# Performance work log

Measured on AMD Instinct MI355X. Metric: run time of the kernel, lower is better.

## Reference

```python
import jax, jax.numpy as jnp
import numpy as np

N, F, H, C, E = 50000, 256, 256, 40, 800000
CURV = 1.0
EPS = 4e-3      # hgcn PoincareBall eps for float32
MIN_NORM = 1e-15


def setup_inputs() -> dict:
    key = jax.random.key(0)
    ks = jax.random.split(key, 8)
    return {
        "x": jax.random.normal(ks[0], (N, F), jnp.float32),
        "edge_index": jax.random.randint(ks[1], (2, E), 0, N, dtype=jnp.int64),
        "Wl0": jax.random.normal(ks[2], (F, H), jnp.float32) / np.sqrt(F).astype(np.float32),
        "bl0": jnp.zeros((H,), jnp.float32),
        "Wr0": jax.random.normal(ks[3], (F, H), jnp.float32) / np.sqrt(F).astype(np.float32),
        "Wl1": jax.random.normal(ks[4], (H, C), jnp.float32) / np.sqrt(H).astype(np.float32),
        "bl1": jnp.zeros((C,), jnp.float32),
        "Wr1": jax.random.normal(ks[5], (H, C), jnp.float32) / np.sqrt(H).astype(np.float32),
        "W_lin": jax.random.normal(ks[6], (C * C, C), jnp.float32) / np.sqrt(C * C).astype(np.float32),
        "b_lin": jnp.zeros((C,), jnp.float32),
    }


def _sage(x, src, dst, Wl, bl, Wr):
    # PyG SAGEConv (mean aggr): lin_l(mean_{j->i} x_j) + lin_r(x_i), lin_l has bias
    msg = jax.ops.segment_sum(x[src], dst, num_segments=N)          # [N, d]
    cnt = jax.ops.segment_sum(jnp.ones((src.shape[0],), x.dtype), dst, num_segments=N)
    mean = msg / jnp.maximum(cnt, 1.0)[:, None]
    return mean @ Wl + bl + x @ Wr


def _proj(x, c):
    norm = jnp.maximum(jnp.linalg.norm(x, axis=-1, keepdims=True), MIN_NORM)
    maxnorm = (1.0 - EPS) / jnp.sqrt(c)
    return jnp.where(norm > maxnorm, x / norm * maxnorm, x)


def _logmap0(p, c):
    sqrt_c = jnp.sqrt(c)
    p_norm = jnp.maximum(jnp.linalg.norm(p, axis=-1, keepdims=True), MIN_NORM)
    arg = jnp.clip(sqrt_c * p_norm, -1.0 + 1e-6, 1.0 - 1e-6)
    return jnp.arctanh(arg) / (sqrt_c * p_norm) * p


def _expmap0(u, c):
    sqrt_c = jnp.sqrt(c)
    u_norm = jnp.maximum(jnp.linalg.norm(u, axis=-1, keepdims=True), MIN_NORM)
    return jnp.tanh(sqrt_c * u_norm) * u / (sqrt_c * u_norm)


def reference(x, edge_index, Wl0, bl0, Wr0, Wl1, bl1, Wr1, W_lin, b_lin):
    c = CURV
    src, dst = edge_index[0], edge_index[1]
    h = jax.nn.relu(_sage(x, src, dst, Wl0, bl0, Wr0))              # [N, H]
    h = _sage(h, src, dst, Wl1, bl1, Wr1)                            # [N, C]
    outer = jnp.einsum('ni,nj->nij', h, h).reshape(N, C * C)        # rank-1 outer, flattened
    h_hyp = _proj(outer, c)
    h_euc = _logmap0(h_hyp, c)                                       # proj_tan0 is identity
    h_euc = h_euc @ W_lin + b_lin                                    # [N, C]
    h_hyp = _proj(_expmap0(h_euc, c), c)
    return jax.nn.log_softmax(h_hyp, axis=-1)
```

## Files before the change

kernel.cpp:

```cpp
#include <hip/hip_runtime.h>
#include <math.h>


typedef short bf16x8 __attribute__((ext_vector_type(8)));
typedef float f32x4 __attribute__((ext_vector_type(4)));

#define AS1 __attribute__((address_space(1)))
#define AS3 __attribute__((address_space(3)))

__device__ inline unsigned pack_bf16_hu(float a, float b) {
    unsigned ua = __float_as_uint(a) + 0x8000u;
    unsigned ub = __float_as_uint(b) + 0x8000u;
    return __builtin_amdgcn_perm(ub, ua, 0x07060302u);
}

__device__ inline unsigned short f2bf_rne(float x) {
    unsigned u = __float_as_uint(x);
    unsigned r = (u + 0x7fffu + ((u >> 16) & 1u)) >> 16;
    return (unsigned short)r;
}

__device__ inline void split2(float a, float b, unsigned* hw, unsigned* lw) {
    unsigned ua = __float_as_uint(a) + 0x8000u;
    unsigned ub = __float_as_uint(b) + 0x8000u;
    *hw = __builtin_amdgcn_perm(ub, ua, 0x07060302u);
    float ra = a - __uint_as_float(ua & 0xFFFF0000u);
    float rb = b - __uint_as_float(ub & 0xFFFF0000u);
    unsigned va = __float_as_uint(ra) + 0x8000u;
    unsigned vb = __float_as_uint(rb) + 0x8000u;
    *lw = __builtin_amdgcn_perm(vb, va, 0x07060302u);
}


__global__ void k_count(const int* __restrict__ dst, int* __restrict__ deg, int E) {
    int e = blockIdx.x * 256 + threadIdx.x;
    if (e < E) atomicAdd(&deg[dst[e]], 1);
}

__global__ __launch_bounds__(256) void k_scanA(const int* __restrict__ deg,
                                               int* __restrict__ offs,
                                               float* __restrict__ invc,
                                               int* __restrict__ bsum, int N) {
    __shared__ int wt[4];
    int tid = threadIdx.x, lane = tid & 63, wid = tid >> 6;
    int base = blockIdx.x * 1024 + tid * 4;
    int v[4];
    #pragma unroll
    for (int j = 0; j < 4; ++j) {
        int i = base + j;
        v[j] = (i < N) ? deg[i] : 0;
        if (i < N) invc[i] = 1.0f / (float)max(v[j], 1);
    }
    int t = v[0] + v[1] + v[2] + v[3];
    int s = t;
    #pragma unroll
    for (int d = 1; d < 64; d <<= 1) {
        int u = __shfl_up(s, d);
        if (lane >= d) s += u;
    }
    if (lane == 63) wt[wid] = s;
    __syncthreads();
    int wpre = 0, btot = 0;
    #pragma unroll
    for (int q = 0; q < 4; ++q) {
        int x = wt[q];
        btot += x;
        if (q < wid) wpre += x;
    }
    int run = wpre + s - t;
    #pragma unroll
    for (int j = 0; j < 4; ++j) {
        int i = base + j;
        if (i < N) offs[i] = run;
        run += v[j];
    }
    if (tid == 0) bsum[blockIdx.x] = btot;
}

__global__ __launch_bounds__(64) void k_scanB(int* __restrict__ bsum,
                                              int* __restrict__ offs, int N, int G) {
    int lane = threadIdx.x;
    int run = 0;
    for (int base = 0; base < G; base += 64) {
        int i = base + lane;
        int v = (i < G) ? bsum[i] : 0;
        int s = v;
        #pragma unroll
        for (int d = 1; d < 64; d <<= 1) {
            int u = __shfl_up(s, d);
            if (lane >= d) s += u;
        }
        int tot = __shfl(s, 63);
        if (i < G) bsum[i] = run + s - v;
        run += tot;
    }
    if (lane == 0) offs[N] = run;
}

__global__ __launch_bounds__(256) void k_scanC(int* __restrict__ offs,
                                               const int* __restrict__ bsum, int N) {
    int add = bsum[blockIdx.x];
    int base = blockIdx.x * 1024 + threadIdx.x * 4;
    #pragma unroll
    for (int j = 0; j < 4; ++j) {
        int i = base + j;
        if (i < N) offs[i] += add;
    }
}

__global__ void k_scatter(const int* __restrict__ src, const int* __restrict__ dst,
                          const int* __restrict__ offs, int* __restrict__ cursor,
                          int* __restrict__ ssrc, int E) {
    int e = blockIdx.x * 256 + threadIdx.x;
    if (e >= E) return;
    int d = dst[e];
    int pos = offs[d] + atomicAdd(&cursor[d], 1);
    ssrc[pos] = src[e];
}


__global__ __launch_bounds__(256) void k_wsplit0(const float* __restrict__ Wl,
                                                 const float* __restrict__ Wr,
                                                 unsigned short* __restrict__ Bfh,
                                                 unsigned short* __restrict__ Bfl) {
    int idx = blockIdx.x * 256 + threadIdx.x;
    int lane = idx & 63;
    int nf = (idx >> 6) & 3;
    int g  = (idx >> 8) & 7;
    int w  = (idx >> 11) & 7;
    int ml = lane & 15, quad = lane >> 4;
    int wc = w & 3;
    int n = (w < 4) ? (wc * 64 + (nf & 2) * 16 + 2 * ml + (nf & 1))
                    : (256 + wc * 64 + nf * 16 + ml);
    int kbase = g * 32 + quad * 8;
    unsigned short h8[8], l8[8];
    #pragma unroll
    for (int e = 0; e < 8; ++e) {
        int k = kbase + e;
        float v = (n < 256) ? Wl[k * 256 + n] : Wr[k * 256 + (n - 256)];
        unsigned short h = f2bf_rne(v);
        float hf = __uint_as_float(((unsigned)h) << 16);
        h8[e] = h;
        l8[e] = f2bf_rne(v - hf);
    }
    *(uint4*)&Bfh[(size_t)idx * 8] = *(uint4*)h8;
    *(uint4*)&Bfl[(size_t)idx * 8] = *(uint4*)l8;
}


__global__ __launch_bounds__(256) void k_wsplit1(const float* __restrict__ Wl,
                                                 const float* __restrict__ Wr,
                                                 unsigned short* __restrict__ Bfh,
                                                 unsigned short* __restrict__ Bfl) {
    int idx = blockIdx.x * 256 + threadIdx.x;
    if (idx >= 40 * 64) return;
    int lane = idx & 63;
    int slot = idx >> 6;
    int nf = slot % 5;
    int kc = slot / 5;
    int ml = lane & 15, quad = lane >> 4;
    int n = nf * 16 + ml;
    int kbase = kc * 32 + quad * 8;
    unsigned short h8[8], l8[8];
    #pragma unroll
    for (int e = 0; e < 8; ++e) {
        int k = kbase + e;
        float v = (n < 40) ? Wl[k * 40 + n] : Wr[k * 40 + (n - 40)];
        unsigned short h = f2bf_rne(v);
        float hf = __uint_as_float(((unsigned)h) << 16);
        h8[e] = h;
        l8[e] = f2bf_rne(v - hf);
    }
    *(uint4*)&Bfh[(size_t)idx * 8] = *(uint4*)h8;
    *(uint4*)&Bfl[(size_t)idx * 8] = *(uint4*)l8;
}


__global__ __launch_bounds__(256) void k_xsplit(const float* __restrict__ X,
                                                unsigned short* __restrict__ Xh,
                                                unsigned short* __restrict__ Xl,
                                                int N) {
    int idx = blockIdx.x * 256 + threadIdx.x;
    int n = idx >> 5, c = idx & 31;
    float4 v0 = make_float4(0.f, 0.f, 0.f, 0.f);
    float4 v1 = make_float4(0.f, 0.f, 0.f, 0.f);
    if (n < N) {
        v0 = *(const float4*)&X[(size_t)n * 256 + c * 8];
        v1 = *(const float4*)&X[(size_t)n * 256 + c * 8 + 4];
    }
    unsigned h0, l0, h1, l1, h2, l2, h3, l3;
    split2(v0.x, v0.y, &h0, &l0);
    split2(v0.z, v0.w, &h1, &l1);
    split2(v1.x, v1.y, &h2, &l2);
    split2(v1.z, v1.w, &h3, &l3);
    int cp = c ^ (n & 7);
    size_t o = (size_t)n * 256 + cp * 8;
    *(uint4*)&Xh[o] = make_uint4(h0, h1, h2, h3);
    *(uint4*)&Xl[o] = make_uint4(l0, l1, l2, l3);
}


__global__ __launch_bounds__(512) void gemm0_mfma(const unsigned short* __restrict__ Xh,
                                                  const unsigned short* __restrict__ Xl,
                                                  const unsigned short* __restrict__ Bfh,
                                                  const unsigned short* __restrict__ Bfl,
                                                  unsigned short* __restrict__ Yl,
                                                  float* __restrict__ Yr, int N) {
    __shared__ __align__(16) unsigned short AhL[2][64 * 128];
    __shared__ __align__(16) unsigned short AlL[2][64 * 128];

    int tid = threadIdx.x;
    int lane = tid & 63;
    int w = __builtin_amdgcn_readfirstlane(tid >> 6);
    int ml = lane & 15, quad = lane >> 4;
    int m0 = blockIdx.x * 64;
    bool isYl = (w < 4);
    int wc = w & 3;

    auto stage = [&](int h) {
        #pragma unroll
        for (int j = 0; j < 2; ++j) {
            int idx = j * 512 + tid;
            int row = idx >> 4, c16 = idx & 15;
            size_t gsrc = (size_t)(m0 + row) * 512 + (size_t)h * 256 + c16 * 16;
            int loff = idx * 16;
            __builtin_amdgcn_global_load_lds((const AS1 unsigned*)((const char*)Xh + gsrc),
                                             (AS3 unsigned*)((char*)&AhL[h][0] + loff), 16, 0, 0);
            __builtin_amdgcn_global_load_lds((const AS1 unsigned*)((const char*)Xl + gsrc),
                                             (AS3 unsigned*)((char*)&AlL[h][0] + loff), 16, 0, 0);
        }
    };

    stage(0);

    f32x4 acc[4][4];
    #pragma unroll
    for (int a = 0; a < 4; ++a)
        #pragma unroll
        for (int b = 0; b < 4; ++b) acc[a][b] = (f32x4){0.f, 0.f, 0.f, 0.f};

    bf16x8 bh0[4], bl0[4], bh1[4], bl1[4];

    auto loadB = [&](int it, bf16x8* bh, bf16x8* bl) {
        size_t base = (((size_t)(w * 8 + it) * 4) * 64 + lane) * 8;
        #pragma unroll
        for (int nf = 0; nf < 4; ++nf) {
            bh[nf] = *(const bf16x8*)&Bfh[base + (size_t)nf * 512];
            bl[nf] = *(const bf16x8*)&Bfl[base + (size_t)nf * 512];
        }
    };

    loadB(0, bh0, bl0);
    __syncthreads();

    int swz = ml & 7;

    #pragma unroll
    for (int p = 0; p < 2; ++p) {
        if (p == 0) stage(1);
        const char* base_h = (const char*)&AhL[p][0];
        const char* base_l = (const char*)&AlL[p][0];
        #pragma unroll
        for (int g2 = 0; g2 < 4; ++g2) {
            int g = p * 4 + g2;
            bf16x8* bhc = (g & 1) ? bh1 : bh0;
            bf16x8* blc = (g & 1) ? bl1 : bl0;
            bf16x8* bhn = (g & 1) ? bh0 : bh1;
            bf16x8* bln = (g & 1) ? bl0 : bl1;
            if (g < 7) loadB(g + 1, bhn, bln);
            bf16x8 ah[4], al[4];
            #pragma unroll
            for (int mf = 0; mf < 4; ++mf) {
                int ro = (mf * 16 + ml) * 256 + (((g2 * 4 + quad) ^ swz) * 16);
                ah[mf] = *(const bf16x8*)(base_h + ro);
                al[mf] = *(const bf16x8*)(base_l + ro);
            }
            #pragma unroll
            for (int nf = 0; nf < 4; ++nf)
                #pragma unroll
                for (int mf = 0; mf < 4; ++mf) {
                    acc[mf][nf] = __builtin_amdgcn_mfma_f32_16x16x32_bf16(ah[mf], bhc[nf], acc[mf][nf], 0, 0, 0);
                    acc[mf][nf] = __builtin_amdgcn_mfma_f32_16x16x32_bf16(ah[mf], blc[nf], acc[mf][nf], 0, 0, 0);
                    acc[mf][nf] = __builtin_amdgcn_mfma_f32_16x16x32_bf16(al[mf], bhc[nf], acc[mf][nf], 0, 0, 0);
                }
        }
        if (p == 0) __syncthreads();
    }

    if (isYl) {
        #pragma unroll
        for (int mf = 0; mf < 4; ++mf)
            #pragma unroll
            for (int r = 0; r < 4; ++r) {
                int row = m0 + mf * 16 + quad * 4 + r;
                if (row < N) {
                    unsigned p0 = pack_bf16_hu(acc[mf][0][r], acc[mf][1][r]);
                    unsigned p1 = pack_bf16_hu(acc[mf][2][r], acc[mf][3][r]);
                    *(unsigned*)&Yl[(size_t)row * 256 + wc * 64 + 2 * ml] = p0;
                    *(unsigned*)&Yl[(size_t)row * 256 + wc * 64 + 32 + 2 * ml] = p1;
                }
            }
    } else {
        #pragma unroll
        for (int mf = 0; mf < 4; ++mf)
            #pragma unroll
            for (int r = 0; r < 4; ++r) {
                int row = m0 + mf * 16 + quad * 4 + r;
                if (row < N) {
                    #pragma unroll
                    for (int nf = 0; nf < 4; ++nf)
                        Yr[(size_t)row * 256 + wc * 64 + nf * 16 + ml] = acc[mf][nf][r];
                }
            }
    }
}


__global__ __launch_bounds__(256) void combine0(const unsigned short* __restrict__ Yl,
                                                const float* __restrict__ Yr,
                                                const int* __restrict__ offs,
                                                const int* __restrict__ ssrc,
                                                const float* __restrict__ invc,
                                                const float* __restrict__ bl0,
                                                unsigned short* __restrict__ Hh,
                                                unsigned short* __restrict__ Hl, int N) {
    int wv = threadIdx.x >> 6, lane = threadIdx.x & 63;
    int n = blockIdx.x * 4 + wv;
    if (n >= N) return;
    int e0 = offs[n], e1 = offs[n + 1];
    float4 acc = make_float4(0.f, 0.f, 0.f, 0.f);
    int e = e0;
    for (; e + 7 < e1; e += 8) {
        int s0 = ssrc[e],     s1 = ssrc[e + 1], s2 = ssrc[e + 2], s3 = ssrc[e + 3];
        int s4 = ssrc[e + 4], s5 = ssrc[e + 5], s6 = ssrc[e + 6], s7 = ssrc[e + 7];
        uint2 p0 = *(const uint2*)&Yl[(size_t)s0 * 256 + lane * 4];
        uint2 p1 = *(const uint2*)&Yl[(size_t)s1 * 256 + lane * 4];
        uint2 p2 = *(const uint2*)&Yl[(size_t)s2 * 256 + lane * 4];
        uint2 p3 = *(const uint2*)&Yl[(size_t)s3 * 256 + lane * 4];
        uint2 p4 = *(const uint2*)&Yl[(size_t)s4 * 256 + lane * 4];
        uint2 p5 = *(const uint2*)&Yl[(size_t)s5 * 256 + lane * 4];
        uint2 p6 = *(const uint2*)&Yl[(size_t)s6 * 256 + lane * 4];
        uint2 p7 = *(const uint2*)&Yl[(size_t)s7 * 256 + lane * 4];
        acc.x += ((__uint_as_float(p0.x << 16) + __uint_as_float(p1.x << 16)) +
                  (__uint_as_float(p2.x << 16) + __uint_as_float(p3.x << 16))) +
                 ((__uint_as_float(p4.x << 16) + __uint_as_float(p5.x << 16)) +
                  (__uint_as_float(p6.x << 16) + __uint_as_float(p7.x << 16)));
        acc.y += ((__uint_as_float(p0.x & 0xFFFF0000u) + __uint_as_float(p1.x & 0xFFFF0000u)) +
                  (__uint_as_float(p2.x & 0xFFFF0000u) + __uint_as_float(p3.x & 0xFFFF0000u))) +
                 ((__uint_as_float(p4.x & 0xFFFF0000u) + __uint_as_float(p5.x & 0xFFFF0000u)) +
                  (__uint_as_float(p6.x & 0xFFFF0000u) + __uint_as_float(p7.x & 0xFFFF0000u)));
        acc.z += ((__uint_as_float(p0.y << 16) + __uint_as_float(p1.y << 16)) +
                  (__uint_as_float(p2.y << 16) + __uint_as_float(p3.y << 16))) +
                 ((__uint_as_float(p4.y << 16) + __uint_as_float(p5.y << 16)) +
                  (__uint_as_float(p6.y << 16) + __uint_as_float(p7.y << 16)));
        acc.w += ((__uint_as_float(p0.y & 0xFFFF0000u) + __uint_as_float(p1.y & 0xFFFF0000u)) +
                  (__uint_as_float(p2.y & 0xFFFF0000u) + __uint_as_float(p3.y & 0xFFFF0000u))) +
                 ((__uint_as_float(p4.y & 0xFFFF0000u) + __uint_as_float(p5.y & 0xFFFF0000u)) +
                  (__uint_as_float(p6.y & 0xFFFF0000u) + __uint_as_float(p7.y & 0xFFFF0000u)));
    }
    for (; e + 3 < e1; e += 4) {
        int s0 = ssrc[e], s1 = ssrc[e + 1], s2 = ssrc[e + 2], s3 = ssrc[e + 3];
        uint2 p = *(const uint2*)&Yl[(size_t)s0 * 256 + lane * 4];
        uint2 q = *(const uint2*)&Yl[(size_t)s1 * 256 + lane * 4];
        uint2 v = *(const uint2*)&Yl[(size_t)s2 * 256 + lane * 4];
        uint2 t = *(const uint2*)&Yl[(size_t)s3 * 256 + lane * 4];
        acc.x += (__uint_as_float(p.x << 16) + __uint_as_float(q.x << 16)) +
                 (__uint_as_float(v.x << 16) + __uint_as_float(t.x << 16));
        acc.y += (__uint_as_float(p.x & 0xFFFF0000u) + __uint_as_float(q.x & 0xFFFF0000u)) +
                 (__uint_as_float(v.x & 0xFFFF0000u) + __uint_as_float(t.x & 0xFFFF0000u));
        acc.z += (__uint_as_float(p.y << 16) + __uint_as_float(q.y << 16)) +
                 (__uint_as_float(v.y << 16) + __uint_as_float(t.y << 16));
        acc.w += (__uint_as_float(p.y & 0xFFFF0000u) + __uint_as_float(q.y & 0xFFFF0000u)) +
                 (__uint_as_float(v.y & 0xFFFF0000u) + __uint_as_float(t.y & 0xFFFF0000u));
    }
    for (; e < e1; ++e) {
        int s0 = ssrc[e];
        uint2 p = *(const uint2*)&Yl[(size_t)s0 * 256 + lane * 4];
        acc.x += __uint_as_float(p.x << 16);
        acc.y += __uint_as_float(p.x & 0xFFFF0000u);
        acc.z += __uint_as_float(p.y << 16);
        acc.w += __uint_as_float(p.y & 0xFFFF0000u);
    }
    float ic = invc[n];
    float4 b = *(const float4*)&bl0[lane * 4];
    float4 yr = *(const float4*)&Yr[(size_t)n * 256 + lane * 4];
    float hx = fmaxf(acc.x * ic + b.x + yr.x, 0.f);
    float hy = fmaxf(acc.y * ic + b.y + yr.y, 0.f);
    float hz = fmaxf(acc.z * ic + b.z + yr.z, 0.f);
    float hw = fmaxf(acc.w * ic + b.w + yr.w, 0.f);
    unsigned h0, h1, l0, l1;
    split2(hx, hy, &h0, &l0);
    split2(hz, hw, &h1, &l1);
    size_t offH = (size_t)n * 256 + lane * 4;
    *(uint2*)&Hh[offH] = make_uint2(h0, h1);
    *(uint2*)&Hl[offH] = make_uint2(l0, l1);
}


__global__ __launch_bounds__(256) void gemm1_mfma(const unsigned short* __restrict__ Hh,
                                                  const unsigned short* __restrict__ Hl,
                                                  const unsigned short* __restrict__ Bfh,
                                                  const unsigned short* __restrict__ Bfl,
                                                  unsigned short* __restrict__ Zl,
                                                  float* __restrict__ Zr, int N, int numTiles) {
    int tid = threadIdx.x;
    int lane = tid & 63;
    int w = __builtin_amdgcn_readfirstlane(tid >> 6);
    int ml = lane & 15, quad = lane >> 4;
    int t = blockIdx.x * 4 + w;
    if (t >= numTiles) return;

    const unsigned short* ahp = Hh + (size_t)(t * 16 + ml) * 256 + quad * 8;
    const unsigned short* alp = Hl + (size_t)(t * 16 + ml) * 256 + quad * 8;

    f32x4 acc[5];
    #pragma unroll
    for (int b = 0; b < 5; ++b) acc[b] = (f32x4){0.f, 0.f, 0.f, 0.f};

    #pragma unroll
    for (int kc = 0; kc < 8; ++kc) {
        bf16x8 ah = *(const bf16x8*)&ahp[kc * 32];
        bf16x8 al = *(const bf16x8*)&alp[kc * 32];
        #pragma unroll
        for (int nf = 0; nf < 5; ++nf) {
            size_t bo = (((size_t)(kc * 5 + nf)) * 64 + lane) * 8;
            bf16x8 bh = *(const bf16x8*)&Bfh[bo];
            bf16x8 bl = *(const bf16x8*)&Bfl[bo];
            acc[nf] = __builtin_amdgcn_mfma_f32_16x16x32_bf16(ah, bh, acc[nf], 0, 0, 0);
            acc[nf] = __builtin_amdgcn_mfma_f32_16x16x32_bf16(ah, bl, acc[nf], 0, 0, 0);
            acc[nf] = __builtin_amdgcn_mfma_f32_16x16x32_bf16(al, bh, acc[nf], 0, 0, 0);
        }
    }
    #pragma unroll
    for (int r = 0; r < 4; ++r) {
        int n = t * 16 + quad * 4 + r;
        if (n < N) {
            #pragma unroll
            for (int nf = 0; nf < 5; ++nf) {
                int col = nf * 16 + ml;
                if (col < 40) Zl[(size_t)n * 40 + col] = f2bf_rne(acc[nf][r]);
                else Zr[(size_t)n * 40 + (col - 40)] = acc[nf][r];
            }
        }
    }
}


__global__ __launch_bounds__(256) void combine1(const unsigned short* __restrict__ Zl,
                                                const float* __restrict__ Zr,
                                                const int* __restrict__ offs,
                                                const int* __restrict__ ssrc,
                                                const float* __restrict__ invc,
                                                const float* __restrict__ bl1,
                                                float* __restrict__ H2, int N) {
    int wv = threadIdx.x >> 6, lane = threadIdx.x & 63;
    int n = blockIdx.x * 4 + wv;
    if (n >= N) return;
    if (lane >= 40) return;
    int e0 = offs[n], e1 = offs[n + 1];
    float acc = 0.f;
    int e = e0;
    for (; e + 1 < e1; e += 2) {
        int s0 = ssrc[e], s1 = ssrc[e + 1];
        unsigned a = Zl[(size_t)s0 * 40 + lane];
        unsigned b = Zl[(size_t)s1 * 40 + lane];
        acc += __uint_as_float(a << 16) + __uint_as_float(b << 16);
    }
    if (e < e1) {
        unsigned a = Zl[(size_t)ssrc[e] * 40 + lane];
        acc += __uint_as_float(a << 16);
    }
    float v = acc * invc[n] + bl1[lane] + Zr[(size_t)n * 40 + lane];
    H2[(size_t)n * 40 + lane] = v;
}


__global__ __launch_bounds__(256) void k_wprep(const float* __restrict__ W,
                                               unsigned short* __restrict__ WbF) {
    int idx = blockIdx.x * 256 + threadIdx.x;
    if (idx >= 180 * 64) return;
    int slot = idx >> 6, lane = idx & 63;
    int cf = slot % 3;
    int cs = slot / 3;
    int s = cs % 3;
    int c = cs / 3;
    int ml = lane & 15, quad = lane >> 4;
    int col = cf * 16 + ml;
    int kbase = c * 96 + s * 32 + quad * 8;
    unsigned short v8[8];
    #pragma unroll
    for (int e = 0; e < 8; ++e) {
        int kp = kbase + e;
        int i = kp / 48;
        int j = kp - i * 48;
        float v = 0.f;
        if (col < 40 && i < 40 && j < 40) v = W[((size_t)(i * 40 + j)) * 40 + col];
        v8[e] = f2bf_rne(v);
    }
    *(uint4*)&WbF[(size_t)idx * 8] = *(uint4*)v8;
}


__global__ __launch_bounds__(256, 1) void k_final_mfma(const float* __restrict__ H2,
                                                       const unsigned short* __restrict__ WbF,
                                                       const float* __restrict__ blin,
                                                       float* __restrict__ out, int N) {
    int tid = threadIdx.x;
    int m0 = blockIdx.x * 64;
    int lane = tid & 63;
    int w = __builtin_amdgcn_readfirstlane(tid >> 6);
    int ml = lane & 15;
    int quad = lane >> 4;
    int row = w * 16 + ml;
    int gn = m0 + row;

    float g[48];
    float s2 = 0.f;
    #pragma unroll
    for (int q4 = 0; q4 < 10; ++q4) {
        float4 v = make_float4(0.f, 0.f, 0.f, 0.f);
        if (gn < N) v = *(const float4*)&H2[(size_t)gn * 40 + q4 * 4];
        g[q4 * 4 + 0] = v.x; g[q4 * 4 + 1] = v.y;
        g[q4 * 4 + 2] = v.z; g[q4 * 4 + 3] = v.w;
        s2 += v.x * v.x + v.y * v.y + v.z * v.z + v.w * v.w;
    }
    #pragma unroll
    for (int j = 40; j < 48; ++j) g[j] = 0.f;

    float aln = atanhf(fminf(fmaxf(s2, 1e-15f), 0.996f)) / fmaxf(s2, 1e-30f);

    bool isQ0 = (quad == 0), isQ2 = (quad == 2), qLo = (quad < 2);
    float wA[8], wB[8], wC[8];
    #pragma unroll
    for (int j = 0; j < 8; ++j) {
        float a0 = isQ0 ? g[j] : g[8 + j];
        float a1 = isQ2 ? g[16 + j] : g[24 + j];
        wA[j] = qLo ? a0 : a1;
        float b0 = isQ0 ? g[32 + j] : g[40 + j];
        float b1 = isQ2 ? g[j] : g[8 + j];
        wB[j] = qLo ? b0 : b1;
        float c0 = isQ0 ? g[16 + j] : g[24 + j];
        float c1 = isQ2 ? g[32 + j] : g[40 + j];
        wC[j] = qLo ? c0 : c1;
    }

    f32x4 acc[3];
    #pragma unroll
    for (int c = 0; c < 3; ++c) acc[c] = (f32x4){0.f, 0.f, 0.f, 0.f};

    const unsigned short* bw = WbF + (size_t)lane * 8;

    #pragma unroll
    for (int c = 0; c < 20; ++c) {
        float gi0 = g[2 * c];
        float gi1 = qLo ? g[2 * c] : g[2 * c + 1];
        float gi2 = g[2 * c + 1];
        {
            const int slot = (c * 3 + 0) * 3;
            union { unsigned u[4]; bf16x8 v; } A;
            A.u[0] = pack_bf16_hu(gi0 * wA[0], gi0 * wA[1]);
            A.u[1] = pack_bf16_hu(gi0 * wA[2], gi0 * wA[3]);
            A.u[2] = pack_bf16_hu(gi0 * wA[4], gi0 * wA[5]);
            A.u[3] = pack_bf16_hu(gi0 * wA[6], gi0 * wA[7]);
            #pragma unroll
            for (int cf = 0; cf < 3; ++cf) {
                bf16x8 bf = *(const bf16x8*)&bw[(size_t)(slot + cf) * 512];
                acc[cf] = __builtin_amdgcn_mfma_f32_16x16x32_bf16(A.v, bf, acc[cf], 0, 0, 0);
            }
        }
        {
            const int slot = (c * 3 + 1) * 3;
            union { unsigned u[4]; bf16x8 v; } A;
            A.u[0] = pack_bf16_hu(gi1 * wB[0], gi1 * wB[1]);
            A.u[1] = pack_bf16_hu(gi1 * wB[2], gi1 * wB[3]);
            A.u[2] = pack_bf16_hu(gi1 * wB[4], gi1 * wB[5]);
            A.u[3] = pack_bf16_hu(gi1 * wB[6], gi1 * wB[7]);
            #pragma unroll
            for (int cf = 0; cf < 3; ++cf) {
                bf16x8 bf = *(const bf16x8*)&bw[(size_t)(slot + cf) * 512];
                acc[cf] = __builtin_amdgcn_mfma_f32_16x16x32_bf16(A.v, bf, acc[cf], 0, 0, 0);
            }
        }
        {
            const int slot = (c * 3 + 2) * 3;
            union { unsigned u[4]; bf16x8 v; } A;
            A.u[0] = pack_bf16_hu(gi2 * wC[0], gi2 * wC[1]);
            A.u[1] = pack_bf16_hu(gi2 * wC[2], gi2 * wC[3]);
            A.u[2] = pack_bf16_hu(gi2 * wC[4], gi2 * wC[5]);
            A.u[3] = pack_bf16_hu(gi2 * wC[6], gi2 * wC[7]);
            #pragma unroll
            for (int cf = 0; cf < 3; ++cf) {
                bf16x8 bf = *(const bf16x8*)&bw[(size_t)(slot + cf) * 512];
                acc[cf] = __builtin_amdgcn_mfma_f32_16x16x32_bf16(A.v, bf, acc[cf], 0, 0, 0);
            }
        }
    }

    float bcol[3];
    #pragma unroll
    for (int c = 0; c < 3; ++c) {
        int col = c * 16 + ml;
        bcol[c] = (col < 40) ? blin[col] : 0.f;
    }
    bool v2 = (ml < 8);

    #pragma unroll
    for (int r = 0; r < 4; ++r) {
        int nloc = w * 16 + quad * 4 + r;
        float al = __shfl(aln, quad * 4 + r);
        float u0 = al * acc[0][r] + bcol[0];
        float u1 = al * acc[1][r] + bcol[1];
        float u2 = v2 ? (al * acc[2][r] + bcol[2]) : 0.f;
        float un2 = u0 * u0 + u1 * u1 + u2 * u2;
        #pragma unroll
        for (int m = 1; m < 16; m <<= 1) un2 += __shfl_xor(un2, m);
        float un = fmaxf(sqrtf(un2), 1e-15f);
        float tnh = tanhf(un);
        float gma = tnh / un;
        float ps = (tnh > 0.996f) ? (0.996f / tnh) : 1.0f;
        float s = gma * ps;
        float l0 = s * u0, l1 = s * u1, l2 = s * u2;
        float mx = fmaxf(l0, l1);
        if (v2) mx = fmaxf(mx, l2);
        #pragma unroll
        for (int m = 1; m < 16; m <<= 1) mx = fmaxf(mx, __shfl_xor(mx, m));
        float se = expf(l0 - mx) + expf(l1 - mx) + (v2 ? expf(l2 - mx) : 0.f);
        #pragma unroll
        for (int m = 1; m < 16; m <<= 1) se += __shfl_xor(se, m);
        float lse = logf(se);
        int go = m0 + nloc;
        if (go < N) {
            out[(size_t)go * 40 + ml] = l0 - mx - lse;
            out[(size_t)go * 40 + 16 + ml] = l1 - mx - lse;
            if (v2) out[(size_t)go * 40 + 32 + ml] = l2 - mx - lse;
        }
    }
}


extern "C" void kernel_launch(void* const* d_in, const int* in_sizes, int n_in,
                              void* d_out, int out_size, void* d_ws, size_t ws_size,
                              hipStream_t stream) {
    const float* x    = (const float*)d_in[0];
    const int*   ei   = (const int*)d_in[1];
    const float* Wl0  = (const float*)d_in[2];
    const float* bl0  = (const float*)d_in[3];
    const float* Wr0  = (const float*)d_in[4];
    const float* Wl1  = (const float*)d_in[5];
    const float* bl1  = (const float*)d_in[6];
    const float* Wr1  = (const float*)d_in[7];
    const float* Wlin = (const float*)d_in[8];
    const float* blin = (const float*)d_in[9];
    int N = in_sizes[0] / 256;
    int E = in_sizes[1] / 2;
    const int* src = ei;
    const int* dst = ei + E;
    int numTiles = (N + 15) / 16;
    int Npad = ((N + 63) / 64) * 64;

    char* ws = (char*)d_ws;
    size_t off = 0;
    auto carve = [&](size_t bytes) -> char* {
        char* p = ws + off;
        off = (off + bytes + 255) & ~(size_t)255;
        return p;
    };
    size_t xbytes = (size_t)Npad * 256 * 2;
    int*   deg    = (int*)carve((size_t)N * 4);
    int*   cursor = (int*)carve((size_t)N * 4);
    int*   offs   = (int*)carve((size_t)(N + 1) * 4);
    float* invc   = (float*)carve((size_t)N * 4);
    int*   bsum   = (int*)carve(1024);
    int*   ssrc   = (int*)carve((size_t)E * 4);
    unsigned short* Yl = (unsigned short*)carve((size_t)N * 256 * 2);
    float* Yr     = (float*)carve((size_t)N * 256 * 4);
    unsigned short* Hh = (unsigned short*)carve(xbytes);
    unsigned short* Hl = (unsigned short*)carve(xbytes);
    unsigned short* Zl = (unsigned short*)carve((size_t)N * 40 * 2);
    float* Zr     = (float*)carve((size_t)N * 40 * 4);
    float* H2     = (float*)carve((size_t)N * 40 * 4);
    unsigned short* Xh = Hh;
    unsigned short* Xl = Hl;
    unsigned short* Wb = (unsigned short*)Yr;
    unsigned short* Wth  = (unsigned short*)H2;
    unsigned short* Wtl  = Wth + 512 * 256;
    unsigned short* Wt1h = Wtl + 512 * 256;
    unsigned short* Wt1l = Wt1h + 80 * 256;

    int G = (N + 1023) / 1024;

    hipMemsetAsync(deg, 0, (size_t)N * 4, stream);
    hipMemsetAsync(cursor, 0, (size_t)N * 4, stream);

    k_count<<<(E + 255) / 256, 256, 0, stream>>>(dst, deg, E);
    k_scanA<<<G, 256, 0, stream>>>(deg, offs, invc, bsum, N);
    k_scanB<<<1, 64, 0, stream>>>(bsum, offs, N, G);
    k_scanC<<<G, 256, 0, stream>>>(offs, bsum, N);
    k_scatter<<<(E + 255) / 256, 256, 0, stream>>>(src, dst, offs, cursor, ssrc, E);
    k_wsplit0<<<64, 256, 0, stream>>>(Wl0, Wr0, Wth, Wtl);
    k_wsplit1<<<(40 * 64 + 255) / 256, 256, 0, stream>>>(Wl1, Wr1, Wt1h, Wt1l);
    k_xsplit<<<(Npad * 32) / 256, 256, 0, stream>>>(x, Xh, Xl, N);
    gemm0_mfma<<<(N + 63) / 64, 512, 0, stream>>>(Xh, Xl, Wth, Wtl, Yl, Yr, N);
    combine0<<<(N + 3) / 4, 256, 0, stream>>>(Yl, Yr, offs, ssrc, invc, bl0, Hh, Hl, N);
    k_wprep<<<(180 * 64 + 255) / 256, 256, 0, stream>>>(Wlin, Wb);
    gemm1_mfma<<<(numTiles + 3) / 4, 256, 0, stream>>>(Hh, Hl, Wt1h, Wt1l, Zl, Zr, N, numTiles);
    combine1<<<(N + 3) / 4, 256, 0, stream>>>(Zl, Zr, offs, ssrc, invc, bl1, H2, N);
    k_final_mfma<<<(N + 63) / 64, 256, 0, stream>>>(H2, Wb, blin, (float*)d_out, N);
}
```

Baseline: 422.0 us.

## Fold scan-block-sum pass into scanC, merge memsets, unroll combine1 gather by eight

Drops the single-wave k_scanB launch. Each scanC block now sums the preceding block totals itself with a wave reduction, and offs[N] is set directly to E. The two memsets for deg and cursor become one memset over a contiguous buffer. combine1's neighbor gather loop is unrolled to eight edges so more loads are in flight at once. Together these cut launch count and serial latency, at the cost of each scanC block redundantly reading up to G block sums.

```diff
diff --git a/kernel.cpp b/kernel.cpp
--- a/kernel.cpp
+++ b/kernel.cpp
@@ -77,35 +77,30 @@
     if (tid == 0) bsum[blockIdx.x] = btot;
 }
 
-__global__ __launch_bounds__(64) void k_scanB(int* __restrict__ bsum,
-                                              int* __restrict__ offs, int N, int G) {
-    int lane = threadIdx.x;
-    int run = 0;
-    for (int base = 0; base < G; base += 64) {
-        int i = base + lane;
-        int v = (i < G) ? bsum[i] : 0;
-        int s = v;
-        #pragma unroll
-        for (int d = 1; d < 64; d <<= 1) {
-            int u = __shfl_up(s, d);
-            if (lane >= d) s += u;
-        }
-        int tot = __shfl(s, 63);
-        if (i < G) bsum[i] = run + s - v;
-        run += tot;
-    }
-    if (lane == 0) offs[N] = run;
-}
 
 __global__ __launch_bounds__(256) void k_scanC(int* __restrict__ offs,
-                                               const int* __restrict__ bsum, int N) {
-    int add = bsum[blockIdx.x];
-    int base = blockIdx.x * 1024 + threadIdx.x * 4;
+                                               const int* __restrict__ bsum,
+                                               int N, int E, int G) {
+    __shared__ int s_add;
+    int tid = threadIdx.x;
+    if (tid < 64) {
+        int bid = blockIdx.x;
+        int v = 0;
+        for (int i = tid; i < G; i += 64)
+            if (i < bid) v += bsum[i];
+        #pragma unroll
+        for (int d = 1; d < 64; d <<= 1) v += __shfl_xor(v, d);
+        if (tid == 0) s_add = v;
+    }
+    __syncthreads();
+    int add = s_add;
+    int base = blockIdx.x * 1024 + tid * 4;
     #pragma unroll
     for (int j = 0; j < 4; ++j) {
         int i = base + j;
         if (i < N) offs[i] += add;
     }
+    if (blockIdx.x == 0 && tid == 0) offs[N] = E;
 }
 
 __global__ void k_scatter(const int* __restrict__ src, const int* __restrict__ dst,
@@ -460,6 +455,22 @@
     int e0 = offs[n], e1 = offs[n + 1];
     float acc = 0.f;
     int e = e0;
+    for (; e + 7 < e1; e += 8) {
+        int s0 = ssrc[e],     s1 = ssrc[e + 1], s2 = ssrc[e + 2], s3 = ssrc[e + 3];
+        int s4 = ssrc[e + 4], s5 = ssrc[e + 5], s6 = ssrc[e + 6], s7 = ssrc[e + 7];
+        unsigned a0 = Zl[(size_t)s0 * 40 + lane];
+        unsigned a1 = Zl[(size_t)s1 * 40 + lane];
+        unsigned a2 = Zl[(size_t)s2 * 40 + lane];
+        unsigned a3 = Zl[(size_t)s3 * 40 + lane];
+        unsigned a4 = Zl[(size_t)s4 * 40 + lane];
+        unsigned a5 = Zl[(size_t)s5 * 40 + lane];
+        unsigned a6 = Zl[(size_t)s6 * 40 + lane];
+        unsigned a7 = Zl[(size_t)s7 * 40 + lane];
+        acc += ((__uint_as_float(a0 << 16) + __uint_as_float(a1 << 16)) +
+                (__uint_as_float(a2 << 16) + __uint_as_float(a3 << 16))) +
+               ((__uint_as_float(a4 << 16) + __uint_as_float(a5 << 16)) +
+                (__uint_as_float(a6 << 16) + __uint_as_float(a7 << 16)));
+    }
     for (; e + 1 < e1; e += 2) {
         int s0 = ssrc[e], s1 = ssrc[e + 1];
         unsigned a = Zl[(size_t)s0 * 40 + lane];
@@ -666,8 +677,8 @@
         return p;
     };
     size_t xbytes = (size_t)Npad * 256 * 2;
-    int*   deg    = (int*)carve((size_t)N * 4);
-    int*   cursor = (int*)carve((size_t)N * 4);
+    int*   deg    = (int*)carve((size_t)(2 * N) * 4);
+    int*   cursor = deg + N;
     int*   offs   = (int*)carve((size_t)(N + 1) * 4);
     float* invc   = (float*)carve((size_t)N * 4);
     int*   bsum   = (int*)carve(1024);
@@ -689,13 +700,11 @@
 
     int G = (N + 1023) / 1024;
 
-    hipMemsetAsync(deg, 0, (size_t)N * 4, stream);
-    hipMemsetAsync(cursor, 0, (size_t)N * 4, stream);
+    hipMemsetAsync(deg, 0, (size_t)(2 * N) * 4, stream);
 
     k_count<<<(E + 255) / 256, 256, 0, stream>>>(dst, deg, E);
     k_scanA<<<G, 256, 0, stream>>>(deg, offs, invc, bsum, N);
-    k_scanB<<<1, 64, 0, stream>>>(bsum, offs, N, G);
-    k_scanC<<<G, 256, 0, stream>>>(offs, bsum, N);
+    k_scanC<<<G, 256, 0, stream>>>(offs, bsum, N, E, G);
     k_scatter<<<(E + 255) / 256, 256, 0, stream>>>(src, dst, offs, cursor, ssrc, E);
     k_wsplit0<<<64, 256, 0, stream>>>(Wl0, Wr0, Wth, Wtl);
     k_wsplit1<<<(40 * 64 + 255) / 256, 256, 0, stream>>>(Wl1, Wr1, Wt1h, Wt1l);
```

Result: faster. 398.8 us, median of 2 (-5.5%).
